# Performance work log

Measured on AMD Instinct MI355X. Metric: run time of the kernel, lower is better.

The kernel has to match this reference:

```python
import jax, jax.numpy as jnp
import numpy as np

N_NODES = 50000
N_EDGES = 800000
IN_CH = 64
HID = 128


def setup_inputs() -> dict:
    key = jax.random.key(0)
    ks = jax.random.split(key, 8)
    s = 0.05
    x = jax.random.normal(ks[0], (N_NODES, IN_CH), dtype=jnp.float32)
    edge_index = jax.random.randint(ks[1], (2, N_EDGES), 0, N_NODES, dtype=jnp.int64)
    return {
        "x": x,
        "edge_index": edge_index,
        "W1l": jax.random.normal(ks[2], (HID, IN_CH), dtype=jnp.float32) * s,
        "b1l": jnp.zeros((HID,), dtype=jnp.float32),
        "W1r": jax.random.normal(ks[3], (HID, IN_CH), dtype=jnp.float32) * s,
        "W2l": jax.random.normal(ks[4], (HID, HID), dtype=jnp.float32) * s,
        "b2l": jnp.zeros((HID,), dtype=jnp.float32),
        "W2r": jax.random.normal(ks[5], (HID, HID), dtype=jnp.float32) * s,
        "Wrec": jax.random.normal(ks[6], (IN_CH, HID), dtype=jnp.float32) * s,
        "brec": jnp.zeros((IN_CH,), dtype=jnp.float32),
    }


def _sage_conv(x, src, dst, Wl, bl, Wr, n_nodes):
    # mean aggregation of source features at destination nodes
    msg_sum = jax.ops.segment_sum(x[src], dst, num_segments=n_nodes)  # [N, d]
    deg = jax.ops.segment_sum(jnp.ones((src.shape[0],), x.dtype), dst,
                              num_segments=n_nodes)  # [N]
    mean = msg_sum / jnp.maximum(deg, 1.0)[:, None]
    # SAGEConv: lin_l(aggr) + lin_r(x_i); lin_l has bias, lin_r does not
    return mean @ Wl.T + bl + x @ Wr.T


def reference(x, edge_index, W1l, b1l, W1r, W2l, b2l, W2r, Wrec, brec):
    src, dst = edge_index[0], edge_index[1]
    n = x.shape[0]
    h = _sage_conv(x, src, dst, W1l, b1l, W1r, n)
    h = jax.nn.relu(h)  # activation between layers, none after last
    z = _sage_conv(h, src, dst, W2l, b2l, W2r, n)
    x_recon = z @ Wrec.T + brec
    return (z, x_recon)
```

## Files before the change

### kernel.cpp

```cpp
#include <hip/hip_runtime.h>

#define N_NODES 50000
#define N_EDGES 800000
#define IN_CH 64
#define HID 128
#define NB_SCAN ((N_NODES + 255) / 256)

typedef short short8 __attribute__((ext_vector_type(8)));
typedef float f32x4 __attribute__((ext_vector_type(4)));

static __device__ __forceinline__ unsigned short f2bf(float f) {
    unsigned u = __float_as_uint(f);
    u += 0x7FFF + ((u >> 16) & 1);
    return (unsigned short)(u >> 16);
}
static __device__ __forceinline__ float bflo(unsigned v) { return __uint_as_float(v << 16); }
static __device__ __forceinline__ float bfhi(unsigned v) { return __uint_as_float(v & 0xFFFF0000u); }


__global__ __launch_bounds__(256) void k_cvt(const float* __restrict__ src,
                                             unsigned short* __restrict__ dst, int n4) {
    int i = blockIdx.x * 256 + threadIdx.x;
    if (i < n4) {
        float4 v = ((const float4*)src)[i];
        unsigned lo = f2bf(v.x) | ((unsigned)f2bf(v.y) << 16);
        unsigned hi = f2bf(v.z) | ((unsigned)f2bf(v.w) << 16);
        ((uint2*)dst)[i] = make_uint2(lo, hi);
    }
}

__global__ __launch_bounds__(256) void k_cvt_w(const float* __restrict__ W1l, const float* __restrict__ W1r,
                                               const float* __restrict__ W2l, const float* __restrict__ W2r,
                                               const float* __restrict__ Wrec, unsigned short* __restrict__ dst) {
    int i = blockIdx.x * 256 + threadIdx.x;
    int e = i * 4;
    if (e >= 57344) return;
    const float* src; int off;
    if (e < 8192)       { src = W1l;  off = 0; }
    else if (e < 16384) { src = W1r;  off = 8192; }
    else if (e < 32768) { src = W2l;  off = 16384; }
    else if (e < 49152) { src = W2r;  off = 32768; }
    else                { src = Wrec; off = 49152; }
    float4 v = *(const float4*)(src + (e - off));
    unsigned lo = f2bf(v.x) | ((unsigned)f2bf(v.y) << 16);
    unsigned hi = f2bf(v.z) | ((unsigned)f2bf(v.w) << 16);
    *(uint2*)(dst + e) = make_uint2(lo, hi);
}


__global__ __launch_bounds__(256) void k_deg(const int* __restrict__ ei, int* __restrict__ deg) {
    int e = blockIdx.x * 256 + threadIdx.x;
    if (e < N_EDGES) {
        int d = ei[N_EDGES + e];
        if ((unsigned)d < N_NODES) atomicAdd(&deg[d], 1);
    }
}

__global__ __launch_bounds__(256) void k_scan1(const int* __restrict__ deg,
                                               int* __restrict__ excl,
                                               int* __restrict__ bsum) {
    int gid = blockIdx.x * 256 + threadIdx.x;
    int v = (gid < N_NODES) ? deg[gid] : 0;
    int lane = threadIdx.x & 63, wv = threadIdx.x >> 6;
    int s = v;
    #pragma unroll
    for (int d = 1; d < 64; d <<= 1) {
        int t = __shfl_up(s, d);
        if (lane >= d) s += t;
    }
    __shared__ int wsum[4];
    if (lane == 63) wsum[wv] = s;
    __syncthreads();
    int add = 0;
    #pragma unroll
    for (int w = 0; w < 4; w++) add += (w < wv) ? wsum[w] : 0;
    s += add;
    if (gid < N_NODES) excl[gid] = s - v;
    if (threadIdx.x == 255) bsum[blockIdx.x] = s;
}

__global__ __launch_bounds__(256) void k_scan2(const int* __restrict__ bsum,
                                               int* __restrict__ bpre,
                                               int* __restrict__ offs) {
    int tid = threadIdx.x;
    int v = (tid < NB_SCAN) ? bsum[tid] : 0;
    int lane = tid & 63, wv = tid >> 6;
    int s = v;
    #pragma unroll
    for (int d = 1; d < 64; d <<= 1) {
        int t = __shfl_up(s, d);
        if (lane >= d) s += t;
    }
    __shared__ int wsum[4];
    if (lane == 63) wsum[wv] = s;
    __syncthreads();
    int add = 0;
    #pragma unroll
    for (int w = 0; w < 4; w++) add += (w < wv) ? wsum[w] : 0;
    s += add;
    if (tid < NB_SCAN) bpre[tid] = s - v;
    if (tid == NB_SCAN - 1) offs[N_NODES] = s;
}

__global__ __launch_bounds__(256) void k_scan3(const int* __restrict__ excl,
                                               const int* __restrict__ bpre,
                                               int* __restrict__ offs) {
    int gid = blockIdx.x * 256 + threadIdx.x;
    if (gid < N_NODES) offs[gid] = excl[gid] + bpre[blockIdx.x];
}

__global__ __launch_bounds__(256) void k_fill(const int* __restrict__ ei, const int* __restrict__ offs,
                                              int* __restrict__ cursor, int* __restrict__ csr) {
    int e = blockIdx.x * 256 + threadIdx.x;
    if (e < N_EDGES) {
        int s = ei[e];
        int d = ei[N_EDGES + e];
        if ((unsigned)d < N_NODES && (unsigned)s < N_NODES) {
            int pos = atomicAdd(&cursor[d], 1);
            csr[offs[d] + pos] = s;
        }
    }
}

__global__ __launch_bounds__(256) void k_agg64b(const unsigned short* __restrict__ X,
                                                const int* __restrict__ csr,
                                                const int* __restrict__ offs,
                                                unsigned short* __restrict__ out) {
    int wid = (blockIdx.x * 256 + threadIdx.x) >> 6;
    int lane = threadIdx.x & 63;
    if (wid >= N_NODES) return;
    int beg = offs[wid], end = offs[wid + 1];
    int degn = end - beg;
    float inv = 1.0f / (float)(degn > 0 ? degn : 1);
    int half = lane >> 5, hl = lane & 31;
    float sx = 0.f, sy = 0.f;
    for (int e = beg + half; e < end; e += 2) {
        int idx = csr[e];
        unsigned v = *(const unsigned*)(X + (size_t)idx * 64 + hl * 2);
        sx += bflo(v); sy += bfhi(v);
    }
    sx += __shfl_xor(sx, 32);
    sy += __shfl_xor(sy, 32);
    if (half == 0) {
        unsigned o = f2bf(sx * inv) | ((unsigned)f2bf(sy * inv) << 16);
        *(unsigned*)(out + (size_t)wid * 64 + hl * 2) = o;
    }
}

__global__ __launch_bounds__(256) void k_agg128b(const unsigned short* __restrict__ X,
                                                 const int* __restrict__ csr,
                                                 const int* __restrict__ offs,
                                                 unsigned short* __restrict__ out) {
    int wid = (blockIdx.x * 256 + threadIdx.x) >> 6;
    int lane = threadIdx.x & 63;
    if (wid >= N_NODES) return;
    int beg = offs[wid], end = offs[wid + 1];
    int degn = end - beg;
    float inv = 1.0f / (float)(degn > 0 ? degn : 1);
    float sx = 0.f, sy = 0.f;
    int e = beg;
    for (; e + 2 <= end; e += 2) {
        int i0 = csr[e], i1 = csr[e + 1];
        unsigned a = *(const unsigned*)(X + (size_t)i0 * 128 + lane * 2);
        unsigned b = *(const unsigned*)(X + (size_t)i1 * 128 + lane * 2);
        sx += bflo(a) + bflo(b);
        sy += bfhi(a) + bfhi(b);
    }
    if (e < end) {
        unsigned a = *(const unsigned*)(X + (size_t)csr[e] * 128 + lane * 2);
        sx += bflo(a); sy += bfhi(a);
    }
    unsigned o = f2bf(sx * inv) | ((unsigned)f2bf(sy * inv) << 16);
    *(unsigned*)(out + (size_t)wid * 128 + lane * 2) = o;
}


template <int NOUT, int KTOT, bool DUAL, bool RELU, bool WF32, bool WBF16>
__global__ __launch_bounds__(256) void k_gemm_mfma(const unsigned short* __restrict__ A0,
                                                   const unsigned short* __restrict__ A1,
                                                   const unsigned short* __restrict__ W0,
                                                   const unsigned short* __restrict__ W1,
                                                   const float* __restrict__ bias,
                                                   float* __restrict__ out,
                                                   unsigned short* __restrict__ outb) {
    constexpr int K1 = DUAL ? KTOT / 2 : KTOT;
    constexpr int NF = NOUT / 16;
    int lane = threadIdx.x & 63;
    int wv = threadIdx.x >> 6;
    int m0 = blockIdx.x * 64 + wv * 16;
    int arow = m0 + (lane & 15);
    if (arow >= N_NODES) arow = N_NODES - 1;
    int kg = lane >> 4;

    f32x4 acc[NF] = {};

    #pragma unroll
    for (int ks = 0; ks < KTOT / 32; ks++) {
        int k0 = ks * 32;
        const unsigned short* Ap; const unsigned short* Wp; int kk;
        if (DUAL && k0 >= K1) { Ap = A1; Wp = W1; kk = k0 - K1; }
        else                  { Ap = A0; Wp = W0; kk = k0; }
        short8 a = *(const short8*)(Ap + (size_t)arow * K1 + kk + kg * 8);
        #pragma unroll
        for (int j = 0; j < NF; j++) {
            short8 b = *(const short8*)(Wp + (size_t)(j * 16 + (lane & 15)) * K1 + kk + kg * 8);
            acc[j] = __builtin_amdgcn_mfma_f32_16x16x32_bf16(a, b, acc[j], 0, 0, 0);
        }
    }

    int col = lane & 15;
    int r0 = (lane >> 4) * 4;
    #pragma unroll
    for (int j = 0; j < NF; j++) {
        float bv = bias[j * 16 + col];
        #pragma unroll
        for (int r = 0; r < 4; r++) {
            int grow = m0 + r0 + r;
            if (grow < N_NODES) {
                float v = acc[j][r] + bv;
                if (RELU) v = fmaxf(v, 0.f);
                if (WF32)  out[(size_t)grow * NOUT + j * 16 + col] = v;
                if (WBF16) outb[(size_t)grow * NOUT + j * 16 + col] = f2bf(v);
            }
        }
    }
}


extern "C" void kernel_launch(void* const* d_in, const int* in_sizes, int n_in,
                              void* d_out, int out_size, void* d_ws, size_t ws_size,
                              hipStream_t stream) {
    const float* x    = (const float*)d_in[0];
    const int*   ei   = (const int*)d_in[1];
    const float* W1l  = (const float*)d_in[2];
    const float* b1l  = (const float*)d_in[3];
    const float* W1r  = (const float*)d_in[4];
    const float* W2l  = (const float*)d_in[5];
    const float* b2l  = (const float*)d_in[6];
    const float* W2r  = (const float*)d_in[7];
    const float* Wrec = (const float*)d_in[8];
    const float* brec = (const float*)d_in[9];

    float* z    = (float*)d_out;
    float* xrec = (float*)d_out + (size_t)N_NODES * HID;

    char* ws = (char*)d_ws;
    int*   deg    = (int*)(ws);
    int*   offs   = (int*)(ws + (256u << 10));
    int*   cursor = (int*)(ws + (512u << 10));
    int*   excl   = (int*)(ws + (768u << 10));
    int*   bsum   = (int*)(ws + (1024u << 10));
    int*   bpre   = (int*)(ws + (1028u << 10));
    int*   csr    = (int*)(ws + (2u << 20));
    unsigned short* wb     = (unsigned short*)(ws + (5632u << 10));
    unsigned short* xb     = (unsigned short*)(ws + (7u  << 20));
    unsigned short* hb     = (unsigned short*)(ws + (14u << 20));
    unsigned short* mean1b = (unsigned short*)(ws + (27u << 20));
    unsigned short* mean2b = (unsigned short*)(ws + (27u << 20));
    unsigned short* zb     = (unsigned short*)(ws + (40u << 20));

    unsigned short* W1lb  = wb;
    unsigned short* W1rb  = wb + 8192;
    unsigned short* W2lb  = wb + 16384;
    unsigned short* W2rb  = wb + 32768;
    unsigned short* Wrecb = wb + 49152;

    hipMemsetAsync(deg, 0, N_NODES * sizeof(int), stream);
    hipMemsetAsync(cursor, 0, N_NODES * sizeof(int), stream);

    int egrid = (N_EDGES + 255) / 256;
    int ngrid = (N_NODES + 63) / 64;

    k_cvt_w<<<56, 256, 0, stream>>>(W1l, W1r, W2l, W2r, Wrec, wb);
    k_cvt<<<(800000 + 255) / 256, 256, 0, stream>>>(x, xb, 800000);

    k_deg<<<egrid, 256, 0, stream>>>(ei, deg);
    k_scan1<<<NB_SCAN, 256, 0, stream>>>(deg, excl, bsum);
    k_scan2<<<1, 256, 0, stream>>>(bsum, bpre, offs);
    k_scan3<<<NB_SCAN, 256, 0, stream>>>(excl, bpre, offs);
    k_fill<<<egrid, 256, 0, stream>>>(ei, offs, cursor, csr);

    k_agg64b<<<N_NODES / 4, 256, 0, stream>>>(xb, csr, offs, mean1b);
    k_gemm_mfma<128, 128, true, true, false, true>
        <<<ngrid, 256, 0, stream>>>(mean1b, xb, W1lb, W1rb, b1l, nullptr, hb);
    k_agg128b<<<N_NODES / 4, 256, 0, stream>>>(hb, csr, offs, mean2b);
    k_gemm_mfma<128, 256, true, false, true, true>
        <<<ngrid, 256, 0, stream>>>(mean2b, hb, W2lb, W2rb, b2l, z, zb);
    k_gemm_mfma<64, 128, false, false, true, false>
        <<<ngrid, 256, 0, stream>>>(zb, nullptr, Wrecb, nullptr, brec, xrec, nullptr);
}
```

Before: 349.6 us.

## Bucket-sort CSR build, column-sliced aggregation, and LDS-staged GEMM weights

Replaces the degree-count, three-pass scan and global atomic fill with a two-level bucket sort. Edges are binned into 64-node buckets, then each bucket is sorted locally using shared-memory atomics, which cuts global atomic contention and kernel launches. Aggregation now runs as several launches that each handle a 32-channel slice with four edge groups per wave, to improve cache locality of the gathers. The GEMM stages weights in swizzled LDS instead of reading them from global memory per MFMA. A fixed bucket capacity (BCAP) risks silently dropping edges if a bucket overflows.

```diff
diff --git a/kernel.cpp b/kernel.cpp
--- a/kernel.cpp
+++ b/kernel.cpp
@@ -4,7 +4,8 @@
 #define N_EDGES 800000
 #define IN_CH 64
 #define HID 128
-#define NB_SCAN ((N_NODES + 255) / 256)
+#define NBKT 782
+#define BCAP 1536
 
 typedef short short8 __attribute__((ext_vector_type(8)));
 typedef float f32x4 __attribute__((ext_vector_type(4)));
@@ -48,42 +49,30 @@
 }
 
 
-__global__ __launch_bounds__(256) void k_deg(const int* __restrict__ ei, int* __restrict__ deg) {
+__global__ __launch_bounds__(256) void k_bfill(const int* __restrict__ ei,
+                                               int* __restrict__ bcur,
+                                               unsigned long long* __restrict__ bbuf) {
     int e = blockIdx.x * 256 + threadIdx.x;
     if (e < N_EDGES) {
+        int s = ei[e];
         int d = ei[N_EDGES + e];
-        if ((unsigned)d < N_NODES) atomicAdd(&deg[d], 1);
-    }
-}
-
-__global__ __launch_bounds__(256) void k_scan1(const int* __restrict__ deg,
-                                               int* __restrict__ excl,
-                                               int* __restrict__ bsum) {
-    int gid = blockIdx.x * 256 + threadIdx.x;
-    int v = (gid < N_NODES) ? deg[gid] : 0;
-    int lane = threadIdx.x & 63, wv = threadIdx.x >> 6;
-    int s = v;
-    #pragma unroll
-    for (int d = 1; d < 64; d <<= 1) {
-        int t = __shfl_up(s, d);
-        if (lane >= d) s += t;
-    }
-    __shared__ int wsum[4];
-    if (lane == 63) wsum[wv] = s;
-    __syncthreads();
-    int add = 0;
-    #pragma unroll
-    for (int w = 0; w < 4; w++) add += (w < wv) ? wsum[w] : 0;
-    s += add;
-    if (gid < N_NODES) excl[gid] = s - v;
-    if (threadIdx.x == 255) bsum[blockIdx.x] = s;
-}
-
-__global__ __launch_bounds__(256) void k_scan2(const int* __restrict__ bsum,
-                                               int* __restrict__ bpre,
-                                               int* __restrict__ offs) {
+        if ((unsigned)d < N_NODES && (unsigned)s < N_NODES) {
+            int b = (unsigned)d >> 6;
+            int pos = atomicAdd(&bcur[b], 1);
+            if (pos < BCAP)
+                bbuf[(size_t)b * BCAP + pos] = (unsigned long long)(unsigned)s |
+                                               ((unsigned long long)(unsigned)d << 32);
+        }
+    }
+}
+
+__global__ __launch_bounds__(1024) void k_bscan(const int* __restrict__ bcur,
+                                                int* __restrict__ bbase,
+                                                int* __restrict__ offs) {
     int tid = threadIdx.x;
-    int v = (tid < NB_SCAN) ? bsum[tid] : 0;
+    int raw = (tid < NBKT) ? bcur[tid] : 0;
+    int v = raw < BCAP ? raw : BCAP;
+    if (tid >= NBKT) v = 0;
     int lane = tid & 63, wv = tid >> 6;
     int s = v;
     #pragma unroll
@@ -91,91 +80,94 @@
         int t = __shfl_up(s, d);
         if (lane >= d) s += t;
     }
-    __shared__ int wsum[4];
+    __shared__ int wsum[16];
     if (lane == 63) wsum[wv] = s;
     __syncthreads();
-    int add = 0;
-    #pragma unroll
-    for (int w = 0; w < 4; w++) add += (w < wv) ? wsum[w] : 0;
-    s += add;
-    if (tid < NB_SCAN) bpre[tid] = s - v;
-    if (tid == NB_SCAN - 1) offs[N_NODES] = s;
-}
-
-__global__ __launch_bounds__(256) void k_scan3(const int* __restrict__ excl,
-                                               const int* __restrict__ bpre,
-                                               int* __restrict__ offs) {
-    int gid = blockIdx.x * 256 + threadIdx.x;
-    if (gid < N_NODES) offs[gid] = excl[gid] + bpre[blockIdx.x];
-}
-
-__global__ __launch_bounds__(256) void k_fill(const int* __restrict__ ei, const int* __restrict__ offs,
-                                              int* __restrict__ cursor, int* __restrict__ csr) {
-    int e = blockIdx.x * 256 + threadIdx.x;
-    if (e < N_EDGES) {
-        int s = ei[e];
-        int d = ei[N_EDGES + e];
-        if ((unsigned)d < N_NODES && (unsigned)s < N_NODES) {
-            int pos = atomicAdd(&cursor[d], 1);
-            csr[offs[d] + pos] = s;
-        }
-    }
-}
-
-__global__ __launch_bounds__(256) void k_agg64b(const unsigned short* __restrict__ X,
+    if (tid < 16) {
+        int w = wsum[tid];
+        #pragma unroll
+        for (int d = 1; d < 16; d <<= 1) {
+            int t = __shfl_up(w, d);
+            if (tid >= d) w += t;
+        }
+        wsum[tid] = w;
+    }
+    __syncthreads();
+    int incl = s + (wv > 0 ? wsum[wv - 1] : 0);
+    if (tid < NBKT) bbase[tid] = incl - v;
+    if (tid == NBKT - 1) offs[N_NODES] = incl;
+}
+
+__global__ __launch_bounds__(256) void k_bcsr(const unsigned long long* __restrict__ bbuf,
+                                              const int* __restrict__ bcur,
+                                              const int* __restrict__ bbase,
+                                              int* __restrict__ offs,
+                                              int* __restrict__ csr) {
+    int b = blockIdx.x;
+    int size = bcur[b]; if (size > BCAP) size = BCAP;
+    int base = bbase[b];
+    __shared__ int lcnt[64];
+    __shared__ int lexcl[64];
+    int tid = threadIdx.x;
+    if (tid < 64) lcnt[tid] = 0;
+    __syncthreads();
+    for (int i = tid; i < size; i += 256) {
+        unsigned long long E = __builtin_nontemporal_load(&bbuf[(size_t)b * BCAP + i]);
+        atomicAdd(&lcnt[(unsigned)(E >> 32) & 63], 1);
+    }
+    __syncthreads();
+    if (tid < 64) {
+        int vv = lcnt[tid];
+        int ss = vv;
+        #pragma unroll
+        for (int d = 1; d < 64; d <<= 1) {
+            int t = __shfl_up(ss, d);
+            if (tid >= d) ss += t;
+        }
+        lexcl[tid] = ss - vv;
+        int node = b * 64 + tid;
+        if (node < N_NODES) offs[node] = base + ss - vv;
+    }
+    __syncthreads();
+    if (tid < 64) lcnt[tid] = lexcl[tid];
+    __syncthreads();
+    for (int i = tid; i < size; i += 256) {
+        unsigned long long E = __builtin_nontemporal_load(&bbuf[(size_t)b * BCAP + i]);
+        int p = atomicAdd(&lcnt[(unsigned)(E >> 32) & 63], 1);
+        csr[base + p] = (int)(unsigned)(E & 0xFFFFFFFFull);
+    }
+}
+
+
+template <int CH>
+__global__ __launch_bounds__(256) void k_agg_cs(const unsigned short* __restrict__ X,
                                                 const int* __restrict__ csr,
                                                 const int* __restrict__ offs,
-                                                unsigned short* __restrict__ out) {
+                                                unsigned short* __restrict__ out,
+                                                int c0) {
     int wid = (blockIdx.x * 256 + threadIdx.x) >> 6;
     int lane = threadIdx.x & 63;
     if (wid >= N_NODES) return;
     int beg = offs[wid], end = offs[wid + 1];
     int degn = end - beg;
     float inv = 1.0f / (float)(degn > 0 ? degn : 1);
-    int half = lane >> 5, hl = lane & 31;
+    int g = lane >> 4, hl = lane & 15;
     float sx = 0.f, sy = 0.f;
-    for (int e = beg + half; e < end; e += 2) {
-        int idx = csr[e];
-        unsigned v = *(const unsigned*)(X + (size_t)idx * 64 + hl * 2);
+    for (int e = beg + g; e < end; e += 4) {
+        int idx = __builtin_nontemporal_load(&csr[e]);
+        unsigned v = *(const unsigned*)(X + (size_t)idx * CH + c0 + hl * 2);
         sx += bflo(v); sy += bfhi(v);
     }
-    sx += __shfl_xor(sx, 32);
-    sy += __shfl_xor(sy, 32);
-    if (half == 0) {
+    sx += __shfl_xor(sx, 16); sy += __shfl_xor(sy, 16);
+    sx += __shfl_xor(sx, 32); sy += __shfl_xor(sy, 32);
+    if (g == 0) {
         unsigned o = f2bf(sx * inv) | ((unsigned)f2bf(sy * inv) << 16);
-        *(unsigned*)(out + (size_t)wid * 64 + hl * 2) = o;
-    }
-}
-
-__global__ __launch_bounds__(256) void k_agg128b(const unsigned short* __restrict__ X,
-                                                 const int* __restrict__ csr,
-                                                 const int* __restrict__ offs,
-                                                 unsigned short* __restrict__ out) {
-    int wid = (blockIdx.x * 256 + threadIdx.x) >> 6;
-    int lane = threadIdx.x & 63;
-    if (wid >= N_NODES) return;
-    int beg = offs[wid], end = offs[wid + 1];
-    int degn = end - beg;
-    float inv = 1.0f / (float)(degn > 0 ? degn : 1);
-    float sx = 0.f, sy = 0.f;
-    int e = beg;
-    for (; e + 2 <= end; e += 2) {
-        int i0 = csr[e], i1 = csr[e + 1];
-        unsigned a = *(const unsigned*)(X + (size_t)i0 * 128 + lane * 2);
-        unsigned b = *(const unsigned*)(X + (size_t)i1 * 128 + lane * 2);
-        sx += bflo(a) + bflo(b);
-        sy += bfhi(a) + bfhi(b);
-    }
-    if (e < end) {
-        unsigned a = *(const unsigned*)(X + (size_t)csr[e] * 128 + lane * 2);
-        sx += bflo(a); sy += bfhi(a);
-    }
-    unsigned o = f2bf(sx * inv) | ((unsigned)f2bf(sy * inv) << 16);
-    *(unsigned*)(out + (size_t)wid * 128 + lane * 2) = o;
-}
-
-
-template <int NOUT, int KTOT, bool DUAL, bool RELU, bool WF32, bool WBF16>
+        *(unsigned*)(out + (size_t)wid * CH + c0 + hl * 2) = o;
+    }
+}
+
+
+template <int NOUT, int K1, bool DUAL, bool RELU, bool WF32, bool WBF16>
 __global__ __launch_bounds__(256) void k_gemm_mfma(const unsigned short* __restrict__ A0,
                                                    const unsigned short* __restrict__ A1,
                                                    const unsigned short* __restrict__ W0,
@@ -183,28 +175,47 @@
                                                    const float* __restrict__ bias,
                                                    float* __restrict__ out,
                                                    unsigned short* __restrict__ outb) {
-    constexpr int K1 = DUAL ? KTOT / 2 : KTOT;
     constexpr int NF = NOUT / 16;
-    int lane = threadIdx.x & 63;
-    int wv = threadIdx.x >> 6;
+    constexpr int NPH = DUAL ? 2 : 1;
+    __shared__ char wlds[NOUT * K1 * 2];
+    int tid = threadIdx.x;
+    int lane = tid & 63;
+    int wv = tid >> 6;
     int m0 = blockIdx.x * 64 + wv * 16;
-    int arow = m0 + (lane & 15);
+    int col16 = lane & 15;
+    int kg = lane >> 4;
+    int arow = m0 + col16;
     if (arow >= N_NODES) arow = N_NODES - 1;
-    int kg = lane >> 4;
 
     f32x4 acc[NF] = {};
 
     #pragma unroll
-    for (int ks = 0; ks < KTOT / 32; ks++) {
-        int k0 = ks * 32;
-        const unsigned short* Ap; const unsigned short* Wp; int kk;
-        if (DUAL && k0 >= K1) { Ap = A1; Wp = W1; kk = k0 - K1; }
-        else                  { Ap = A0; Wp = W0; kk = k0; }
-        short8 a = *(const short8*)(Ap + (size_t)arow * K1 + kk + kg * 8);
-        #pragma unroll
-        for (int j = 0; j < NF; j++) {
-            short8 b = *(const short8*)(Wp + (size_t)(j * 16 + (lane & 15)) * K1 + kk + kg * 8);
-            acc[j] = __builtin_amdgcn_mfma_f32_16x16x32_bf16(a, b, acc[j], 0, 0, 0);
+    for (int ph = 0; ph < NPH; ph++) {
+        const unsigned short* Wp = ph ? W1 : W0;
+        const unsigned short* Ap = ph ? A1 : A0;
+        if (ph) __syncthreads();
+        constexpr int CHUNKS = NOUT * K1 / 8;
+        #pragma unroll
+        for (int it = 0; it < CHUNKS / 256; it++) {
+            int ci = tid + it * 256;
+            int j = ci / (K1 / 8);
+            int c = (ci % (K1 / 8)) * 8;
+            short8 w = *(const short8*)(Wp + (size_t)j * K1 + c);
+            int byte = ((j * K1 + c) * 2) ^ ((j & 7) << 4);
+            *(short8*)(wlds + byte) = w;
+        }
+        __syncthreads();
+        #pragma unroll
+        for (int ks = 0; ks < K1 / 32; ks++) {
+            int kk = ks * 32;
+            short8 a = *(const short8*)(Ap + (size_t)arow * K1 + kk + kg * 8);
+            #pragma unroll
+            for (int j = 0; j < NF; j++) {
+                int row = j * 16 + col16;
+                int byte = ((row * K1 + kk + kg * 8) * 2) ^ ((row & 7) << 4);
+                short8 b = *(const short8*)(wlds + byte);
+                acc[j] = __builtin_amdgcn_mfma_f32_16x16x32_bf16(a, b, acc[j], 0, 0, 0);
+            }
         }
     }
 
@@ -245,19 +256,17 @@
     float* xrec = (float*)d_out + (size_t)N_NODES * HID;
 
     char* ws = (char*)d_ws;
-    int*   deg    = (int*)(ws);
-    int*   offs   = (int*)(ws + (256u << 10));
-    int*   cursor = (int*)(ws + (512u << 10));
-    int*   excl   = (int*)(ws + (768u << 10));
-    int*   bsum   = (int*)(ws + (1024u << 10));
-    int*   bpre   = (int*)(ws + (1028u << 10));
-    int*   csr    = (int*)(ws + (2u << 20));
-    unsigned short* wb     = (unsigned short*)(ws + (5632u << 10));
-    unsigned short* xb     = (unsigned short*)(ws + (7u  << 20));
-    unsigned short* hb     = (unsigned short*)(ws + (14u << 20));
-    unsigned short* mean1b = (unsigned short*)(ws + (27u << 20));
-    unsigned short* mean2b = (unsigned short*)(ws + (27u << 20));
-    unsigned short* zb     = (unsigned short*)(ws + (40u << 20));
+    int*   bcur  = (int*)(ws);
+    int*   bbase = (int*)(ws + (4u << 10));
+    int*   offs  = (int*)(ws + (16u << 10));
+    int*   csr   = (int*)(ws + (512u << 10));
+    unsigned long long* bbuf = (unsigned long long*)(ws + (4u << 20));
+    unsigned short* zb     = (unsigned short*)(ws + (4u << 20));
+    unsigned short* mean1b = (unsigned short*)(ws + (17u << 20));
+    unsigned short* mean2b = (unsigned short*)(ws + (17u << 20));
+    unsigned short* wb     = (unsigned short*)(ws + (30u << 20));
+    unsigned short* xb     = (unsigned short*)(ws + (31u << 20));
+    unsigned short* hb     = (unsigned short*)(ws + (38u << 20));
 
     unsigned short* W1lb  = wb;
     unsigned short* W1rb  = wb + 8192;
@@ -265,26 +274,26 @@
     unsigned short* W2rb  = wb + 32768;
     unsigned short* Wrecb = wb + 49152;
 
-    hipMemsetAsync(deg, 0, N_NODES * sizeof(int), stream);
-    hipMemsetAsync(cursor, 0, N_NODES * sizeof(int), stream);
+    (void)hipMemsetAsync(bcur, 0, NBKT * sizeof(int), stream);
 
     int egrid = (N_EDGES + 255) / 256;
     int ngrid = (N_NODES + 63) / 64;
+    int agrid = N_NODES / 4;
 
     k_cvt_w<<<56, 256, 0, stream>>>(W1l, W1r, W2l, W2r, Wrec, wb);
     k_cvt<<<(800000 + 255) / 256, 256, 0, stream>>>(x, xb, 800000);
 
-    k_deg<<<egrid, 256, 0, stream>>>(ei, deg);
-    k_scan1<<<NB_SCAN, 256, 0, stream>>>(deg, excl, bsum);
-    k_scan2<<<1, 256, 0, stream>>>(bsum, bpre, offs);
-    k_scan3<<<NB_SCAN, 256, 0, stream>>>(excl, bpre, offs);
-    k_fill<<<egrid, 256, 0, stream>>>(ei, offs, cursor, csr);
-
-    k_agg64b<<<N_NODES / 4, 256, 0, stream>>>(xb, csr, offs, mean1b);
-    k_gemm_mfma<128, 128, true, true, false, true>
+    k_bfill<<<egrid, 256, 0, stream>>>(ei, bcur, bbuf);
+    k_bscan<<<1, 1024, 0, stream>>>(bcur, bbase, offs);
+    k_bcsr<<<NBKT, 256, 0, stream>>>(bbuf, bcur, bbase, offs, csr);
+
+    for (int c = 0; c < 64; c += 32)
+        k_agg_cs<64><<<agrid, 256, 0, stream>>>(xb, csr, offs, mean1b, c);
+    k_gemm_mfma<128, 64, true, true, false, true>
         <<<ngrid, 256, 0, stream>>>(mean1b, xb, W1lb, W1rb, b1l, nullptr, hb);
-    k_agg128b<<<N_NODES / 4, 256, 0, stream>>>(hb, csr, offs, mean2b);
-    k_gemm_mfma<128, 256, true, false, true, true>
+    for (int c = 0; c < 128; c += 32)
+        k_agg_cs<128><<<agrid, 256, 0, stream>>>(hb, csr, offs, mean2b, c);
+    k_gemm_mfma<128, 128, true, false, true, true>
         <<<ngrid, 256, 0, stream>>>(mean2b, hb, W2lb, W2rb, b2l, z, zb);
     k_gemm_mfma<64, 128, false, false, true, false>
         <<<ngrid, 256, 0, stream>>>(zb, nullptr, Wrecb, nullptr, brec, xrec, nullptr);
```

After: 528.1 us. 1.51x slower.
